# Kernel tuning notes

Measured on AMD Instinct MI355X. Metric: run time of the kernel, lower is better.

## Reference

```python
import jax, jax.numpy as jnp
import numpy as np
from jax import lax

HEAD_NUM = 16
QKV_DIM = 16
TOP_K = 2
SQRT_EMBED = 16.0   # sqrt_embedding_dim for E=256
LOGIT_CLIP = 10.0


def setup_inputs() -> dict:
    key = jax.random.key(0)
    ks = jax.random.split(key, 12)
    B, P, N1, E, HD, NE = 256, 100, 101, 256, 256, 8
    s = 0.05
    return {
        "encoded_last_node": jax.random.normal(ks[0], (B, P, E), jnp.float32),
        "attr": jax.random.uniform(ks[1], (B, P, 4), jnp.float32),
        "encoded_nodes": jax.random.normal(ks[2], (B, N1, E), jnp.float32),
        "ninf_mask": jnp.zeros((B, P, N1), jnp.float32),
        "attention_bias": jax.random.normal(ks[3], (B, P, N1), jnp.float32),
        "attention_bias1": jax.random.normal(ks[4], (B, P, N1), jnp.float32),
        "Wq_last": jax.random.normal(ks[5], (E + 4, HD), jnp.float32) * s,
        "Wk": jax.random.normal(ks[6], (E, HD), jnp.float32) * s,
        "Wv": jax.random.normal(ks[7], (E, HD), jnp.float32) * s,
        "Wg": jax.random.normal(ks[8], (HD, NE), jnp.float32) * s,
        "expert_W": jax.random.normal(ks[9], (NE, HD, E), jnp.float32) * s,
        "expert_b": jnp.zeros((NE, E), jnp.float32),
    }


def _heads(x, H, D):
    B, n, _ = x.shape
    return x.reshape(B, n, H, D).transpose(0, 2, 1, 3)  # (B,H,n,D)


def reference(encoded_last_node, attr, encoded_nodes, ninf_mask,
              attention_bias, attention_bias1, Wq_last, Wk, Wv,
              Wg, expert_W, expert_b):
    B, P, E = encoded_last_node.shape
    H, D = HEAD_NUM, QKV_DIM
    # q from [last_node ; attr], k/v from encoded_nodes (set_kv)
    q = _heads(jnp.concatenate([encoded_last_node, attr], axis=-1) @ Wq_last, H, D)
    k = _heads(encoded_nodes @ Wk, H, D)   # (B,H,N+1,D)
    v = _heads(encoded_nodes @ Wv, H, D)
    inv_sqrt_d = 1.0 / jnp.sqrt(jnp.asarray(D, jnp.float32))
    score = jnp.einsum('bhpd,bhnd->bhpn', q, k) * inv_sqrt_d
    score = score + ninf_mask[:, None, :, :]           # rank3 ninf mask
    w = jax.nn.softmax(score, axis=-1)
    out = jnp.einsum('bhpn,bhnd->bhpd', w, v)
    out_concat = out.transpose(0, 2, 1, 3).reshape(B, P, H * D)
    # --- top-k gated MoE combine (node-level routing, eval path) ---
    x = out_concat.reshape(B * P, H * D)               # tokens
    logits = x @ Wg                                    # (T, NE)
    top_v, top_i = lax.top_k(logits, TOP_K)
    top_g = jax.nn.softmax(top_v, axis=-1)
    gates = jnp.zeros_like(logits).at[
        jnp.arange(x.shape[0])[:, None], top_i].set(top_g)   # (T, NE)
    expert_out = jnp.einsum('tf,efo->teo', x, expert_W) + expert_b[None]
    mh = jnp.einsum('teo,te->to', expert_out, gates).reshape(B, P, E)
    # --- single-head pointer scores with bias + tanh clipping ---
    score2 = jnp.einsum('bpe,bne->bpn', mh, encoded_nodes)
    score2 = score2 + attention_bias + attention_bias1
    score2 = LOGIT_CLIP * jnp.tanh(score2 / SQRT_EMBED)
    probs = jax.nn.softmax(score2 + ninf_mask, axis=-1)  # (B,P,N+1)
    return probs
```

## Files before the change

### kernel.cpp

```cpp
#include <hip/hip_runtime.h>
#include <hip/hip_bf16.h>

#define B   256
#define P   100
#define N1  101
#define E   256
#define HD  256
#define H   16
#define D   16
#define NE  8
#define NTOK (B*P)
#define NKV  (B*N1)

typedef __attribute__((ext_vector_type(8))) short short8;
typedef __attribute__((ext_vector_type(4))) float f32x4;
typedef unsigned short ushort_t;

__device__ __forceinline__ unsigned short f2bf(float f) {
  unsigned int u = __float_as_uint(f);
  unsigned int r = (u + 0x7fffu + ((u >> 16) & 1u)) >> 16;
  return (unsigned short)r;
}
__device__ __forceinline__ float bf2f(unsigned short b) {
  return __uint_as_float(((unsigned int)b) << 16);
}

__global__ __launch_bounds__(256) void wsplit3_kernel(
    const float* __restrict__ W, uint4* __restrict__ Wp, int Kreal) {
  const int gid = blockIdx.x * 256 + threadIdx.x;
  const int lane = gid & 63;
  const int rest = gid >> 6;
  const int gct = rest & 15;
  const int kt = rest >> 4;
  const int k0 = kt * 32 + (lane >> 4) * 8;
  const int c = gct * 16 + (lane & 15);
  unsigned int hw[4], mw[4], lw[4];
#pragma unroll
  for (int jj = 0; jj < 4; ++jj) {
    int ka = k0 + 2 * jj, kb = ka + 1;
    float va = (ka < Kreal) ? W[(size_t)ka * 256 + c] : 0.f;
    float vb = (kb < Kreal) ? W[(size_t)kb * 256 + c] : 0.f;
    unsigned short ha = f2bf(va), hb = f2bf(vb);
    float ra = va - bf2f(ha), rb = vb - bf2f(hb);
    unsigned short ma = f2bf(ra), mb = f2bf(rb);
    unsigned short la = f2bf(ra - bf2f(ma)), lb = f2bf(rb - bf2f(mb));
    hw[jj] = (unsigned int)ha | ((unsigned int)hb << 16);
    mw[jj] = (unsigned int)ma | ((unsigned int)mb << 16);
    lw[jj] = (unsigned int)la | ((unsigned int)lb << 16);
  }
  uint4 uh, um, ul;
  uh.x = hw[0]; uh.y = hw[1]; uh.z = hw[2]; uh.w = hw[3];
  um.x = mw[0]; um.y = mw[1]; um.z = mw[2]; um.w = mw[3];
  ul.x = lw[0]; ul.y = lw[1]; ul.z = lw[2]; ul.w = lw[3];
  Wp[(size_t)(rest * 3 + 0) * 64 + lane] = uh;
  Wp[(size_t)(rest * 3 + 1) * 64 + lane] = um;
  Wp[(size_t)(rest * 3 + 2) * 64 + lane] = ul;
}

__device__ __forceinline__ void split3_pack(const float* v, uint4& uh,
                                            uint4& um, uint4& ul) {
  unsigned int hw[4], mw[4], lw[4];
#pragma unroll
  for (int jj = 0; jj < 4; ++jj) {
    float va = v[2 * jj], vb = v[2 * jj + 1];
    unsigned short ha = f2bf(va), hb = f2bf(vb);
    float ra = va - bf2f(ha), rb = vb - bf2f(hb);
    unsigned short ma = f2bf(ra), mb = f2bf(rb);
    unsigned short la = f2bf(ra - bf2f(ma)), lb = f2bf(rb - bf2f(mb));
    hw[jj] = (unsigned int)ha | ((unsigned int)hb << 16);
    mw[jj] = (unsigned int)ma | ((unsigned int)mb << 16);
    lw[jj] = (unsigned int)la | ((unsigned int)lb << 16);
  }
  uh.x = hw[0]; uh.y = hw[1]; uh.z = hw[2]; uh.w = hw[3];
  um.x = mw[0]; um.y = mw[1]; um.z = mw[2]; um.w = mw[3];
  ul.x = lw[0]; ul.y = lw[1]; ul.z = lw[2]; ul.w = lw[3];
}

__global__ __launch_bounds__(256) void kvproj3_kernel(
    const float* __restrict__ enc, const uint4* __restrict__ Wk3,
    const uint4* __restrict__ Wv3, float* __restrict__ kout,
    float* __restrict__ vout) {
  const int KT = 8;
  const int NKG = KT * 4;
  const int RSTRIDE = KT * 12 + 1;
  __shared__ uint4 als[32 * 97];
  const int tid = threadIdx.x;
  const int row0 = blockIdx.x * 32;
  for (int i = tid; i < 32 * NKG; i += 256) {
    const int row = i >> 5;
    const int kg = i & 31;
    float v[8];
    const float4* s = (const float4*)(enc + (size_t)(row0 + row) * 256 + kg * 8);
    float4 x0 = s[0], x1 = s[1];
    v[0] = x0.x; v[1] = x0.y; v[2] = x0.z; v[3] = x0.w;
    v[4] = x1.x; v[5] = x1.y; v[6] = x1.z; v[7] = x1.w;
    uint4 uh, um, ul;
    split3_pack(v, uh, um, ul);
    const int slot = row * RSTRIDE + kg;
    als[slot] = uh;
    als[slot + NKG] = um;
    als[slot + 2 * NKG] = ul;
  }
  __syncthreads();
  const int w = tid >> 6;
  const int lane = tid & 63;
  const int lr = lane & 15;
  const int lg4 = lane >> 4;
  f32x4 acck[2][4], accv[2][4];
#pragma unroll
  for (int rt = 0; rt < 2; ++rt)
#pragma unroll
    for (int ct = 0; ct < 4; ++ct) {
      acck[rt][ct] = (f32x4){0.f, 0.f, 0.f, 0.f};
      accv[rt][ct] = (f32x4){0.f, 0.f, 0.f, 0.f};
    }
  for (int kt = 0; kt < KT; ++kt) {
    short8 ah[2], am[2], al[2];
#pragma unroll
    for (int rt = 0; rt < 2; ++rt) {
      const int base = (rt * 16 + lr) * RSTRIDE + kt * 4 + lg4;
      ah[rt] = __builtin_bit_cast(short8, als[base]);
      am[rt] = __builtin_bit_cast(short8, als[base + NKG]);
      al[rt] = __builtin_bit_cast(short8, als[base + 2 * NKG]);
    }
#pragma unroll
    for (int ct = 0; ct < 4; ++ct) {
      const int gct = w * 4 + ct;
      const size_t base = (size_t)((kt * 16 + gct) * 3) * 64 + lane;
      {
        short8 bh = __builtin_bit_cast(short8, Wk3[base]);
        short8 bm = __builtin_bit_cast(short8, Wk3[base + 64]);
        short8 bl = __builtin_bit_cast(short8, Wk3[base + 128]);
#pragma unroll
        for (int rt = 0; rt < 2; ++rt) {
          f32x4 a = acck[rt][ct];
          a = __builtin_amdgcn_mfma_f32_16x16x32_bf16(ah[rt], bh, a, 0, 0, 0);
          a = __builtin_amdgcn_mfma_f32_16x16x32_bf16(ah[rt], bm, a, 0, 0, 0);
          a = __builtin_amdgcn_mfma_f32_16x16x32_bf16(am[rt], bh, a, 0, 0, 0);
          a = __builtin_amdgcn_mfma_f32_16x16x32_bf16(am[rt], bm, a, 0, 0, 0);
          a = __builtin_amdgcn_mfma_f32_16x16x32_bf16(ah[rt], bl, a, 0, 0, 0);
          a = __builtin_amdgcn_mfma_f32_16x16x32_bf16(al[rt], bh, a, 0, 0, 0);
          acck[rt][ct] = a;
        }
      }
      {
        short8 bh = __builtin_bit_cast(short8, Wv3[base]);
        short8 bm = __builtin_bit_cast(short8, Wv3[base + 64]);
        short8 bl = __builtin_bit_cast(short8, Wv3[base + 128]);
#pragma unroll
        for (int rt = 0; rt < 2; ++rt) {
          f32x4 a = accv[rt][ct];
          a = __builtin_amdgcn_mfma_f32_16x16x32_bf16(ah[rt], bh, a, 0, 0, 0);
          a = __builtin_amdgcn_mfma_f32_16x16x32_bf16(ah[rt], bm, a, 0, 0, 0);
          a = __builtin_amdgcn_mfma_f32_16x16x32_bf16(am[rt], bh, a, 0, 0, 0);
          a = __builtin_amdgcn_mfma_f32_16x16x32_bf16(am[rt], bm, a, 0, 0, 0);
          a = __builtin_amdgcn_mfma_f32_16x16x32_bf16(ah[rt], bl, a, 0, 0, 0);
          a = __builtin_amdgcn_mfma_f32_16x16x32_bf16(al[rt], bh, a, 0, 0, 0);
          accv[rt][ct] = a;
        }
      }
    }
  }
#pragma unroll
  for (int rt = 0; rt < 2; ++rt) {
#pragma unroll
    for (int ct = 0; ct < 4; ++ct) {
      const int gct = w * 4 + ct;
#pragma unroll
      for (int reg = 0; reg < 4; ++reg) {
        const int row = row0 + rt * 16 + lg4 * 4 + reg;
        int bb = row / N1, nn = row - bb * N1;
        size_t o = (((size_t)bb * H + gct) * N1 + nn) * D + lr;
        kout[o] = acck[rt][ct][reg];
        vout[o] = accv[rt][ct][reg];
      }
    }
  }
}

template <int KT, int MODE>
__global__ __launch_bounds__(256) void proj3_kernel(
    const float* __restrict__ src, const float* __restrict__ attr,
    const uint4* __restrict__ Wp3, float* __restrict__ outp) {
  const int RSTRIDE = KT * 12 + 1;
  __shared__ uint4 als[32 * (KT * 12 + 1)];
  const int tid = threadIdx.x;
  const int row0 = blockIdx.x * 32;
  const int NKG = KT * 4;
  for (int i = tid; i < 32 * NKG; i += 256) {
    const int row = i / NKG;
    const int kg = i - row * NKG;
    float v[8];
    const int kbase = kg * 8;
    if (MODE == 0 || kbase < 256) {
      const float4* s = (const float4*)(src + (size_t)(row0 + row) * 256 + kbase);
      float4 x0 = s[0], x1 = s[1];
      v[0] = x0.x; v[1] = x0.y; v[2] = x0.z; v[3] = x0.w;
      v[4] = x1.x; v[5] = x1.y; v[6] = x1.z; v[7] = x1.w;
    } else {
#pragma unroll
      for (int j = 0; j < 8; ++j) {
        int k = kbase + j;
        v[j] = (k >= 256 && k < 260) ? attr[(size_t)(row0 + row) * 4 + (k - 256)]
                                     : 0.f;
      }
    }
    uint4 uh, um, ul;
    split3_pack(v, uh, um, ul);
    const int slot = row * RSTRIDE + kg;
    als[slot] = uh;
    als[slot + NKG] = um;
    als[slot + 2 * NKG] = ul;
  }
  __syncthreads();
  const int w = tid >> 6;
  const int lane = tid & 63;
  const int lr = lane & 15;
  const int lg4 = lane >> 4;
  f32x4 acc[2][4];
#pragma unroll
  for (int rt = 0; rt < 2; ++rt)
#pragma unroll
    for (int ct = 0; ct < 4; ++ct) acc[rt][ct] = (f32x4){0.f, 0.f, 0.f, 0.f};
  for (int kt = 0; kt < KT; ++kt) {
    short8 ah[2], am[2], al[2];
#pragma unroll
    for (int rt = 0; rt < 2; ++rt) {
      const int base = (rt * 16 + lr) * RSTRIDE + kt * 4 + lg4;
      ah[rt] = __builtin_bit_cast(short8, als[base]);
      am[rt] = __builtin_bit_cast(short8, als[base + NKG]);
      al[rt] = __builtin_bit_cast(short8, als[base + 2 * NKG]);
    }
#pragma unroll
    for (int ct = 0; ct < 4; ++ct) {
      const int gct = w * 4 + ct;
      const size_t base = (size_t)((kt * 16 + gct) * 3) * 64 + lane;
      short8 bh = __builtin_bit_cast(short8, Wp3[base]);
      short8 bm = __builtin_bit_cast(short8, Wp3[base + 64]);
      short8 bl = __builtin_bit_cast(short8, Wp3[base + 128]);
#pragma unroll
      for (int rt = 0; rt < 2; ++rt) {
        f32x4 a = acc[rt][ct];
        a = __builtin_amdgcn_mfma_f32_16x16x32_bf16(ah[rt], bh, a, 0, 0, 0);
        a = __builtin_amdgcn_mfma_f32_16x16x32_bf16(ah[rt], bm, a, 0, 0, 0);
        a = __builtin_amdgcn_mfma_f32_16x16x32_bf16(am[rt], bh, a, 0, 0, 0);
        a = __builtin_amdgcn_mfma_f32_16x16x32_bf16(am[rt], bm, a, 0, 0, 0);
        a = __builtin_amdgcn_mfma_f32_16x16x32_bf16(ah[rt], bl, a, 0, 0, 0);
        a = __builtin_amdgcn_mfma_f32_16x16x32_bf16(al[rt], bh, a, 0, 0, 0);
        acc[rt][ct] = a;
      }
    }
  }
#pragma unroll
  for (int rt = 0; rt < 2; ++rt) {
#pragma unroll
    for (int ct = 0; ct < 4; ++ct) {
      const int gct = w * 4 + ct;
#pragma unroll
      for (int reg = 0; reg < 4; ++reg) {
        const int row = row0 + rt * 16 + lg4 * 4 + reg;
        size_t o;
        if (MODE == 0) {
          int bb = row / N1, nn = row - bb * N1;
          o = (((size_t)bb * H + gct) * N1 + nn) * D + lr;
        } else {
          int bb = row / P, pp = row - bb * P;
          o = (((size_t)bb * H + gct) * P + pp) * D + lr;
        }
        outp[o] = acc[rt][ct][reg];
      }
    }
  }
}

__device__ __forceinline__ float dot16f(
    const float4& a0, const float4& a1, const float4& a2, const float4& a3,
    const float4& b0, const float4& b1, const float4& b2, const float4& b3) {
  float s = a0.x * b0.x;
  s = fmaf(a0.y, b0.y, s); s = fmaf(a0.z, b0.z, s); s = fmaf(a0.w, b0.w, s);
  s = fmaf(a1.x, b1.x, s); s = fmaf(a1.y, b1.y, s); s = fmaf(a1.z, b1.z, s);
  s = fmaf(a1.w, b1.w, s);
  s = fmaf(a2.x, b2.x, s); s = fmaf(a2.y, b2.y, s); s = fmaf(a2.z, b2.z, s);
  s = fmaf(a2.w, b2.w, s);
  s = fmaf(a3.x, b3.x, s); s = fmaf(a3.y, b3.y, s); s = fmaf(a3.z, b3.z, s);
  s = fmaf(a3.w, b3.w, s);
  return s;
}

__global__ __launch_bounds__(256) void attn_kernel(
    const float* __restrict__ q, const float* __restrict__ k,
    const float* __restrict__ v, const float* __restrict__ ninf,
    float* __restrict__ x) {
  const int b = blockIdx.x >> 3;
  const int h0 = (blockIdx.x & 7) * 2;
  __shared__ float4 kl4[2 * 208];
  __shared__ float4 vl4[2 * 208];
  const int tid = threadIdx.x;
  const int w = tid >> 6;
  const int lane = tid & 63;
  const int hh = w >> 1;
  const int h = h0 + hh;
  const int prow = (w & 1) * 64 + lane;
  const bool act = (prow < P);
  const int p = act ? prow : (P - 1);
  const float LOG2E = 1.4426950408889634f;
  const float c1 = 0.25f * LOG2E;
  const float* qb = q + (((size_t)b * H + h) * P + p) * D;
  float4 qa0 = *(const float4*)&qb[0];
  float4 qa1 = *(const float4*)&qb[4];
  float4 qa2 = *(const float4*)&qb[8];
  float4 qa3 = *(const float4*)&qb[12];
  qa0.x *= c1; qa0.y *= c1; qa0.z *= c1; qa0.w *= c1;
  qa1.x *= c1; qa1.y *= c1; qa1.z *= c1; qa1.w *= c1;
  qa2.x *= c1; qa2.y *= c1; qa2.z *= c1; qa2.w *= c1;
  qa3.x *= c1; qa3.y *= c1; qa3.z *= c1; qa3.w *= c1;
  const float* mrow = ninf + ((size_t)b * P + p) * N1;
  const float* kw = (const float*)(kl4 + hh * 208);
  const float* vw = (const float*)(vl4 + hh * 208);

  float m2 = -1e30f, l = 0.f;
  float o[16];
#pragma unroll
  for (int d = 0; d < 16; ++d) o[d] = 0.f;

#pragma unroll
  for (int ch = 0; ch < 2; ++ch) {
    const int c0 = ch ? 52 : 0;
    const int len = ch ? 49 : 52;
    const int nf4 = len * 4;
    __syncthreads();
    for (int i = tid; i < 2 * nf4; i += 256) {
      int hs = i / nf4, rem = i - hs * nf4;
      const float4* ks =
          (const float4*)(k + (((size_t)b * H + h0 + hs) * N1 + c0) * D);
      const float4* vs =
          (const float4*)(v + (((size_t)b * H + h0 + hs) * N1 + c0) * D);
      kl4[hs * 208 + rem] = ks[rem];
      vl4[hs * 208 + rem] = vs[rem];
    }
    __syncthreads();
    const int nit = len >> 2;
    float4 mk = *(const float4*)&mrow[c0];
    for (int it = 0; it < nit; ++it) {
      const int j = it * 4;
      const int nn = (it < nit - 1) ? (c0 + j + 4) : c0;
      float4 nx = *(const float4*)&mrow[nn];
      const float4* kr0 = (const float4*)&kw[(j + 0) * D];
      const float4* kr1 = (const float4*)&kw[(j + 1) * D];
      const float4* kr2 = (const float4*)&kw[(j + 2) * D];
      const float4* kr3 = (const float4*)&kw[(j + 3) * D];
      float4 k00 = kr0[0], k01 = kr0[1], k02 = kr0[2], k03 = kr0[3];
      float4 k10 = kr1[0], k11 = kr1[1], k12 = kr1[2], k13 = kr1[3];
      float4 k20 = kr2[0], k21 = kr2[1], k22 = kr2[2], k23 = kr2[3];
      float4 k30 = kr3[0], k31 = kr3[1], k32 = kr3[2], k33 = kr3[3];
      float s0 = fmaf(mk.x, LOG2E, dot16f(qa0, qa1, qa2, qa3, k00, k01, k02, k03));
      float s1 = fmaf(mk.y, LOG2E, dot16f(qa0, qa1, qa2, qa3, k10, k11, k12, k13));
      float s2 = fmaf(mk.z, LOG2E, dot16f(qa0, qa1, qa2, qa3, k20, k21, k22, k23));
      float s3 = fmaf(mk.w, LOG2E, dot16f(qa0, qa1, qa2, qa3, k30, k31, k32, k33));
      float mn = fmaxf(fmaxf(fmaxf(s0, s1), fmaxf(s2, s3)), m2);
      float sc = exp2f(m2 - mn);
      float p0 = exp2f(s0 - mn), p1 = exp2f(s1 - mn);
      float p2 = exp2f(s2 - mn), p3 = exp2f(s3 - mn);
      l = fmaf(l, sc, (p0 + p1) + (p2 + p3));
      const float4* vr0 = (const float4*)&vw[(j + 0) * D];
      const float4* vr1 = (const float4*)&vw[(j + 1) * D];
      const float4* vr2 = (const float4*)&vw[(j + 2) * D];
      const float4* vr3 = (const float4*)&vw[(j + 3) * D];
#pragma unroll
      for (int dq = 0; dq < 4; ++dq) {
        float4 v0 = vr0[dq], v1 = vr1[dq], v2 = vr2[dq], v3 = vr3[dq];
        o[4 * dq + 0] = fmaf(o[4 * dq + 0], sc,
            fmaf(p0, v0.x, fmaf(p1, v1.x, fmaf(p2, v2.x, p3 * v3.x))));
        o[4 * dq + 1] = fmaf(o[4 * dq + 1], sc,
            fmaf(p0, v0.y, fmaf(p1, v1.y, fmaf(p2, v2.y, p3 * v3.y))));
        o[4 * dq + 2] = fmaf(o[4 * dq + 2], sc,
            fmaf(p0, v0.z, fmaf(p1, v1.z, fmaf(p2, v2.z, p3 * v3.z))));
        o[4 * dq + 3] = fmaf(o[4 * dq + 3], sc,
            fmaf(p0, v0.w, fmaf(p1, v1.w, fmaf(p2, v2.w, p3 * v3.w))));
      }
      m2 = mn;
      mk = nx;
    }
  }
  {
    const float tm = mrow[100];
    const float4* kr = (const float4*)&kw[48 * D];
    float4 k0 = kr[0], k1 = kr[1], k2 = kr[2], k3 = kr[3];
    float s = fmaf(tm, LOG2E, dot16f(qa0, qa1, qa2, qa3, k0, k1, k2, k3));
    float mn = fmaxf(m2, s);
    float sc = exp2f(m2 - mn);
    float pp = exp2f(s - mn);
    l = fmaf(l, sc, pp);
    const float4* vr = (const float4*)&vw[48 * D];
#pragma unroll
    for (int dq = 0; dq < 4; ++dq) {
      float4 v0 = vr[dq];
      o[4 * dq + 0] = fmaf(o[4 * dq + 0], sc, pp * v0.x);
      o[4 * dq + 1] = fmaf(o[4 * dq + 1], sc, pp * v0.y);
      o[4 * dq + 2] = fmaf(o[4 * dq + 2], sc, pp * v0.z);
      o[4 * dq + 3] = fmaf(o[4 * dq + 3], sc, pp * v0.w);
    }
  }
  if (act) {
    const float inv = 1.f / l;
    float* xr = &x[((size_t)b * P + p) * HD + h * D];
#pragma unroll
    for (int dq = 0; dq < 4; ++dq) {
      float4 t;
      t.x = o[4 * dq + 0] * inv; t.y = o[4 * dq + 1] * inv;
      t.z = o[4 * dq + 2] * inv; t.w = o[4 * dq + 3] * inv;
      *(float4*)&xr[4 * dq] = t;
    }
  }
}

__global__ __launch_bounds__(256) void logits_top2_kernel(
    const float* __restrict__ x, const float* __restrict__ Wg,
    int* __restrict__ topi, float* __restrict__ topg,
    ushort_t* __restrict__ xsplit) {
  __shared__ float xl[32][260];
  __shared__ float wg[E * NE];
  __shared__ float lg[32][9];
  const int tid = threadIdx.x;
  const int t0 = blockIdx.x * 32;
  for (int r = 0; r < 32; ++r) {
    float val = x[(size_t)(t0 + r) * HD + tid];
    xl[r][tid] = val;
    unsigned short hi = f2bf(val);
    unsigned short lo = f2bf(val - bf2f(hi));
    xsplit[(size_t)(t0 + r) * 512 + tid] = hi;
    xsplit[(size_t)(t0 + r) * 512 + 256 + tid] = lo;
  }
  for (int i = tid; i < E * NE; i += 256) wg[i] = Wg[i];
  __syncthreads();
  const int r = tid >> 3, e = tid & 7;
  float acc = 0.f;
  for (int f = 0; f < E; ++f) acc += xl[r][f] * wg[f * NE + e];
  lg[r][e] = acc;
  __syncthreads();
  if (tid < 32) {
    float v[8];
#pragma unroll
    for (int j = 0; j < 8; ++j) v[j] = lg[tid][j];
    int i1 = 0; float v1 = v[0];
#pragma unroll
    for (int j = 1; j < 8; ++j) if (v[j] > v1) { v1 = v[j]; i1 = j; }
    int i2 = -1; float v2 = -1e30f;
#pragma unroll
    for (int j = 0; j < 8; ++j)
      if (j != i1 && v[j] > v2) { v2 = v[j]; i2 = j; }
    float ex = __expf(v2 - v1);
    float g1 = 1.f / (1.f + ex);
    float g2 = ex / (1.f + ex);
    int t = t0 + tid;
    topi[t * 2 + 0] = i1; topi[t * 2 + 1] = i2;
    topg[t * 2 + 0] = g1; topg[t * 2 + 1] = g2;
  }
}

__global__ __launch_bounds__(1024) void build_lists_kernel(
    const int* __restrict__ topi, const float* __restrict__ topg,
    int* __restrict__ list_tok, float* __restrict__ list_gate,
    int* __restrict__ counts) {
  const int e = blockIdx.x;
  const int tid = threadIdx.x;
  const int lane = tid & 63, w = tid >> 6;
  __shared__ int wsum[16];
  int running = 0;
  for (int c = 0; c < NTOK; c += 1024) {
    int t = c + tid;
    int ia = topi[t * 2 + 0], ib = topi[t * 2 + 1];
    int slot = (ia == e) ? 0 : ((ib == e) ? 1 : -1);
    int f = (slot >= 0) ? 1 : 0;
    unsigned long long m = __ballot(f);
    if (lane == 0) wsum[w] = __popcll(m);
    __syncthreads();
    int wbase = 0, total = 0;
#pragma unroll
    for (int i = 0; i < 16; ++i) {
      int s = wsum[i];
      if (i < w) wbase += s;
      total += s;
    }
    if (f) {
      int prefix = __popcll(m & ((1ull << lane) - 1ull));
      int pos = running + wbase + prefix;
      list_tok[e * NTOK + pos] = (t << 1) | slot;
      list_gate[e * NTOK + pos] = topg[t * 2 + slot];
    }
    running += total;
    __syncthreads();
  }
  if (tid == 0) counts[e] = running;
}

__global__ __launch_bounds__(256) void wsplit_kernel(
    const float* __restrict__ eW, uint4* __restrict__ Wp) {
  const int gid = blockIdx.x * 256 + threadIdx.x;
  const int lane = gid & 63;
  const int rest = gid >> 6;
  const int gct = rest & 15;
  const int kt = (rest >> 4) & 7;
  const int e = rest >> 7;
  const int kbase = kt * 32 + (lane >> 4) * 8;
  const int c = gct * 16 + (lane & 15);
  unsigned int hi[4], lo[4];
#pragma unroll
  for (int jj = 0; jj < 4; ++jj) {
    float v0 = eW[((size_t)e * HD + (kbase + 2 * jj)) * E + c];
    float v1 = eW[((size_t)e * HD + (kbase + 2 * jj + 1)) * E + c];
    unsigned short h0 = f2bf(v0), h1 = f2bf(v1);
    unsigned short l0 = f2bf(v0 - bf2f(h0)), l1 = f2bf(v1 - bf2f(h1));
    hi[jj] = (unsigned int)h0 | ((unsigned int)h1 << 16);
    lo[jj] = (unsigned int)l0 | ((unsigned int)l1 << 16);
  }
  uint4 uh, ul;
  uh.x = hi[0]; uh.y = hi[1]; uh.z = hi[2]; uh.w = hi[3];
  ul.x = lo[0]; ul.y = lo[1]; ul.z = lo[2]; ul.w = lo[3];
  Wp[(size_t)(rest * 2 + 0) * 64 + lane] = uh;
  Wp[(size_t)(rest * 2 + 1) * 64 + lane] = ul;
}

__global__ __launch_bounds__(256) void expert_gemm_kernel(
    const ushort_t* __restrict__ xsplit, const uint4* __restrict__ Wp,
    const float* __restrict__ eb, const int* __restrict__ list_tok,
    const float* __restrict__ list_gate, const int* __restrict__ counts,
    float* __restrict__ p0, float* __restrict__ p1) {
  int e = 0, t0 = -1;
  {
    int rem = blockIdx.x;
    for (int i = 0; i < NE; ++i) {
      int nt = (counts[i] + 31) >> 5;
      if (rem < nt) { e = i; t0 = rem * 32; break; }
      rem -= nt;
    }
  }
  if (t0 < 0) return;
  const int cnt = counts[e];
  const int nr = min(32, cnt - t0);
  __shared__ uint4 xls[32 * 65];
  __shared__ int stok[32];
  __shared__ float sg[32];
  const int tid = threadIdx.x;
  if (tid < 32) {
    int src = e * NTOK + t0 + ((tid < nr) ? tid : 0);
    stok[tid] = list_tok[src];
    sg[tid] = (tid < nr) ? list_gate[e * NTOK + t0 + tid] : 0.f;
  }
  __syncthreads();
  for (int i = tid; i < 32 * 64; i += 256) {
    int r = i >> 6, ch = i & 63;
    const uint4* src = (const uint4*)(xsplit + (size_t)(stok[r] >> 1) * 512);
    xls[r * 65 + ch] = src[ch];
  }
  __syncthreads();
  const int w = tid >> 6;
  const int lane = tid & 63;
  const int lr = lane & 15;
  const int lg4 = lane >> 4;
  f32x4 acc[2][4];
#pragma unroll
  for (int rt = 0; rt < 2; ++rt)
#pragma unroll
    for (int ct = 0; ct < 4; ++ct) acc[rt][ct] = (f32x4){0.f, 0.f, 0.f, 0.f};

  for (int kt = 0; kt < 8; ++kt) {
    short8 afrag[2][2];
#pragma unroll
    for (int rt = 0; rt < 2; ++rt)
#pragma unroll
      for (int pl = 0; pl < 2; ++pl) {
        uint4 u = xls[(rt * 16 + lr) * 65 + pl * 32 + kt * 4 + lg4];
        afrag[rt][pl] = __builtin_bit_cast(short8, u);
      }
#pragma unroll
    for (int ct = 0; ct < 4; ++ct) {
      const int gct = w * 4 + ct;
      const size_t base = (size_t)(((e * 8 + kt) * 16 + gct) * 2) * 64 + lane;
      short8 bh = __builtin_bit_cast(short8, Wp[base]);
      short8 bl = __builtin_bit_cast(short8, Wp[base + 64]);
#pragma unroll
      for (int rt = 0; rt < 2; ++rt) {
        acc[rt][ct] = __builtin_amdgcn_mfma_f32_16x16x32_bf16(
            afrag[rt][0], bh, acc[rt][ct], 0, 0, 0);
        acc[rt][ct] = __builtin_amdgcn_mfma_f32_16x16x32_bf16(
            afrag[rt][0], bl, acc[rt][ct], 0, 0, 0);
        acc[rt][ct] = __builtin_amdgcn_mfma_f32_16x16x32_bf16(
            afrag[rt][1], bh, acc[rt][ct], 0, 0, 0);
      }
    }
  }
#pragma unroll
  for (int rt = 0; rt < 2; ++rt) {
#pragma unroll
    for (int ct = 0; ct < 4; ++ct) {
      const int col = (w * 4 + ct) * 16 + lr;
      const float bias = eb[e * E + col];
#pragma unroll
      for (int reg = 0; reg < 4; ++reg) {
        const int ridx = rt * 16 + lg4 * 4 + reg;
        if (ridx < nr) {
          const int tokw = stok[ridx];
          const float g = sg[ridx];
          float* dst = ((tokw & 1) ? p1 : p0) + (size_t)(tokw >> 1) * E + col;
          *dst = g * (acc[rt][ct][reg] + bias);
        }
      }
    }
  }
}

__global__ __launch_bounds__(128) void score2_kernel(
    const float* __restrict__ p0, const float* __restrict__ p1,
    const float* __restrict__ enc, float* __restrict__ out) {
  const int b = blockIdx.y;
  const int pt = blockIdx.x * 25;
  __shared__ float mh[25][E];
  const int tid = threadIdx.x;
  for (int i = tid; i < 25 * E; i += 128) {
    int r = i >> 8, c = i & 255;
    int t = b * P + pt + r;
    mh[r][c] = p0[(size_t)t * E + c] + p1[(size_t)t * E + c];
  }
  __syncthreads();
  const int n = tid;
  if (n >= N1) return;
  float acc[25];
#pragma unroll
  for (int r = 0; r < 25; ++r) acc[r] = 0.f;
  const float* er = enc + ((size_t)b * N1 + n) * E;
  for (int ee = 0; ee < E; ee += 4) {
    float4 ev = *(const float4*)&er[ee];
#pragma unroll
    for (int r = 0; r < 25; ++r) {
      float4 mv = *(const float4*)&mh[r][ee];
      acc[r] += mv.x * ev.x + mv.y * ev.y + mv.z * ev.z + mv.w * ev.w;
    }
  }
#pragma unroll
  for (int r = 0; r < 25; ++r) out[((size_t)b * P + pt + r) * N1 + n] = acc[r];
}

__global__ __launch_bounds__(256) void softmax2_kernel(
    float* __restrict__ sc, const float* __restrict__ ab,
    const float* __restrict__ ab1, const float* __restrict__ ninf) {
  const int row = blockIdx.x * 4 + (threadIdx.x >> 6);
  const int lane = threadIdx.x & 63;
  float* srow = sc + (size_t)row * N1;
  const float* a = ab + (size_t)row * N1;
  const float* a1 = ab1 + (size_t)row * N1;
  const float* nf = ninf + (size_t)row * N1;
  float s0 = -1e30f, s1 = -1e30f;
  {
    int i = lane;
    float s = srow[i] + a[i] + a1[i];
    float e2 = __expf(s * 0.125f);
    float th = 1.f - 2.f / (e2 + 1.f);
    s0 = 10.f * th + nf[i];
  }
  if (lane < N1 - 64) {
    int i = lane + 64;
    float s = srow[i] + a[i] + a1[i];
    float e2 = __expf(s * 0.125f);
    float th = 1.f - 2.f / (e2 + 1.f);
    s1 = 10.f * th + nf[i];
  }
  float mx = fmaxf(s0, s1);
#pragma unroll
  for (int off = 32; off > 0; off >>= 1) mx = fmaxf(mx, __shfl_xor(mx, off, 64));
  float p0 = __expf(s0 - mx);
  float p1 = (lane < N1 - 64) ? __expf(s1 - mx) : 0.f;
  float sum = p0 + p1;
#pragma unroll
  for (int off = 32; off > 0; off >>= 1) sum += __shfl_xor(sum, off, 64);
  float inv = 1.f / sum;
  srow[lane] = p0 * inv;
  if (lane < N1 - 64) srow[lane + 64] = p1 * inv;
}

extern "C" void kernel_launch(void* const* d_in, const int* in_sizes, int n_in,
                              void* d_out, int out_size, void* d_ws,
                              size_t ws_size, hipStream_t stream) {
  const float* eln  = (const float*)d_in[0];
  const float* attr = (const float*)d_in[1];
  const float* enc  = (const float*)d_in[2];
  const float* ninf = (const float*)d_in[3];
  const float* ab   = (const float*)d_in[4];
  const float* ab1  = (const float*)d_in[5];
  const float* Wq   = (const float*)d_in[6];
  const float* Wk   = (const float*)d_in[7];
  const float* Wv   = (const float*)d_in[8];
  const float* Wg   = (const float*)d_in[9];
  const float* eW   = (const float*)d_in[10];
  const float* eb   = (const float*)d_in[11];
  float* out = (float*)d_out;

  char* ws = (char*)d_ws;
  size_t off = 0;
  auto carve = [&](size_t bytes) {
    char* p = ws + off;
    off += (bytes + 255) & ~size_t(255);
    return p;
  };
  float* kbuf = (float*)carve(sizeof(float) * NKV * HD);
  float* vbuf = (float*)carve(sizeof(float) * NKV * HD);
  float* qbuf = (float*)carve(sizeof(float) * NTOK * HD);
  float* xbuf = (float*)carve(sizeof(float) * NTOK * HD);
  int*   topi = (int*)carve(sizeof(int) * NTOK * 2);
  float* topg = (float*)carve(sizeof(float) * NTOK * 2);
  int*   counts = (int*)carve(sizeof(int) * 16);
  int*   list_tok = (int*)carve(sizeof(int) * NE * NTOK);
  float* list_gate = (float*)carve(sizeof(float) * NE * NTOK);
  uint4* Wp  = (uint4*)carve(sizeof(ushort_t) * NE * HD * E * 2);
  uint4* Wk3 = (uint4*)carve((size_t)8 * 16 * 3 * 64 * 16);
  uint4* Wv3 = (uint4*)carve((size_t)8 * 16 * 3 * 64 * 16);
  uint4* Wq3 = (uint4*)carve((size_t)9 * 16 * 3 * 64 * 16);
  float* pp0 = kbuf;
  float* pp1 = vbuf;
  ushort_t* xsplit = (ushort_t*)qbuf;

  wsplit_kernel<<<256, 256, 0, stream>>>(eW, Wp);
  wsplit3_kernel<<<32, 256, 0, stream>>>(Wk, Wk3, 256);
  wsplit3_kernel<<<32, 256, 0, stream>>>(Wv, Wv3, 256);
  wsplit3_kernel<<<36, 256, 0, stream>>>(Wq, Wq3, 260);
  kvproj3_kernel<<<NKV / 32, 256, 0, stream>>>(enc, Wk3, Wv3, kbuf, vbuf);
  proj3_kernel<9, 1><<<NTOK / 32, 256, 0, stream>>>(eln, attr, Wq3, qbuf);
  attn_kernel<<<B * 8, 256, 0, stream>>>(qbuf, kbuf, vbuf, ninf, xbuf);
  logits_top2_kernel<<<NTOK / 32, 256, 0, stream>>>(xbuf, Wg, topi, topg,
                                                    xsplit);
  build_lists_kernel<<<NE, 1024, 0, stream>>>(topi, topg, list_tok, list_gate,
                                              counts);
  expert_gemm_kernel<<<1608, 256, 0, stream>>>(xsplit, Wp, eb, list_tok,
                                               list_gate, counts, pp0, pp1);
  dim3 s2(4, B);
  score2_kernel<<<s2, 128, 0, stream>>>(pp0, pp1, enc, out);
  softmax2_kernel<<<NTOK / 4, 256, 0, stream>>>(out, ab, ab1, ninf);
}
```

Baseline: 327.1 us.

## Use hardware bf16 pack conversion and load full K/V into shared memory once

Replaces the software round-to-nearest bf16 split with the v_cvt_pk_bf16_f32 instruction in the weight and activation split helpers. In attention, all 101 K/V rows for both heads are staged into LDS at once, replacing the two-chunk load with its extra barriers. Hardware conversion cuts ALU work per split. Single staging removes a sync and a reload at the cost of roughly double the LDS per block, which may lower occupancy.

```diff
diff --git a/kernel.cpp b/kernel.cpp
--- a/kernel.cpp
+++ b/kernel.cpp
@@ -24,6 +24,35 @@
 __device__ __forceinline__ float bf2f(unsigned short b) {
   return __uint_as_float(((unsigned int)b) << 16);
 }
+__device__ __forceinline__ unsigned int cvtpk(float a, float b) {
+  unsigned int r;
+  asm("v_cvt_pk_bf16_f32 %0, %1, %2" : "=v"(r) : "v"(a), "v"(b));
+  return r;
+}
+__device__ __forceinline__ float lo2f(unsigned int u) {
+  return __uint_as_float(u << 16);
+}
+__device__ __forceinline__ float hi2f(unsigned int u) {
+  return __uint_as_float(u & 0xffff0000u);
+}
+
+__device__ __forceinline__ void split3_pack(const float* v, uint4& uh,
+                                            uint4& um, uint4& ul) {
+  unsigned int hw[4], mw[4], lw[4];
+#pragma unroll
+  for (int jj = 0; jj < 4; ++jj) {
+    float va = v[2 * jj], vb = v[2 * jj + 1];
+    unsigned int h = cvtpk(va, vb);
+    float ra = va - lo2f(h), rb = vb - hi2f(h);
+    unsigned int m = cvtpk(ra, rb);
+    float sa = ra - lo2f(m), sb = rb - hi2f(m);
+    unsigned int l = cvtpk(sa, sb);
+    hw[jj] = h; mw[jj] = m; lw[jj] = l;
+  }
+  uh.x = hw[0]; uh.y = hw[1]; uh.z = hw[2]; uh.w = hw[3];
+  um.x = mw[0]; um.y = mw[1]; um.z = mw[2]; um.w = mw[3];
+  ul.x = lw[0]; ul.y = lw[1]; ul.z = lw[2]; ul.w = lw[3];
+}
 
 __global__ __launch_bounds__(256) void wsplit3_kernel(
     const float* __restrict__ W, uint4* __restrict__ Wp, int Kreal) {
@@ -34,46 +63,17 @@
   const int kt = rest >> 4;
   const int k0 = kt * 32 + (lane >> 4) * 8;
   const int c = gct * 16 + (lane & 15);
-  unsigned int hw[4], mw[4], lw[4];
-#pragma unroll
-  for (int jj = 0; jj < 4; ++jj) {
-    int ka = k0 + 2 * jj, kb = ka + 1;
-    float va = (ka < Kreal) ? W[(size_t)ka * 256 + c] : 0.f;
-    float vb = (kb < Kreal) ? W[(size_t)kb * 256 + c] : 0.f;
-    unsigned short ha = f2bf(va), hb = f2bf(vb);
-    float ra = va - bf2f(ha), rb = vb - bf2f(hb);
-    unsigned short ma = f2bf(ra), mb = f2bf(rb);
-    unsigned short la = f2bf(ra - bf2f(ma)), lb = f2bf(rb - bf2f(mb));
-    hw[jj] = (unsigned int)ha | ((unsigned int)hb << 16);
-    mw[jj] = (unsigned int)ma | ((unsigned int)mb << 16);
-    lw[jj] = (unsigned int)la | ((unsigned int)lb << 16);
+  float v[8];
+#pragma unroll
+  for (int j = 0; j < 8; ++j) {
+    int kk = k0 + j;
+    v[j] = (kk < Kreal) ? W[(size_t)kk * 256 + c] : 0.f;
   }
   uint4 uh, um, ul;
-  uh.x = hw[0]; uh.y = hw[1]; uh.z = hw[2]; uh.w = hw[3];
-  um.x = mw[0]; um.y = mw[1]; um.z = mw[2]; um.w = mw[3];
-  ul.x = lw[0]; ul.y = lw[1]; ul.z = lw[2]; ul.w = lw[3];
+  split3_pack(v, uh, um, ul);
   Wp[(size_t)(rest * 3 + 0) * 64 + lane] = uh;
   Wp[(size_t)(rest * 3 + 1) * 64 + lane] = um;
   Wp[(size_t)(rest * 3 + 2) * 64 + lane] = ul;
-}
-
-__device__ __forceinline__ void split3_pack(const float* v, uint4& uh,
-                                            uint4& um, uint4& ul) {
-  unsigned int hw[4], mw[4], lw[4];
-#pragma unroll
-  for (int jj = 0; jj < 4; ++jj) {
-    float va = v[2 * jj], vb = v[2 * jj + 1];
-    unsigned short ha = f2bf(va), hb = f2bf(vb);
-    float ra = va - bf2f(ha), rb = vb - bf2f(hb);
-    unsigned short ma = f2bf(ra), mb = f2bf(rb);
-    unsigned short la = f2bf(ra - bf2f(ma)), lb = f2bf(rb - bf2f(mb));
-    hw[jj] = (unsigned int)ha | ((unsigned int)hb << 16);
-    mw[jj] = (unsigned int)ma | ((unsigned int)mb << 16);
-    lw[jj] = (unsigned int)la | ((unsigned int)lb << 16);
-  }
-  uh.x = hw[0]; uh.y = hw[1]; uh.z = hw[2]; uh.w = hw[3];
-  um.x = mw[0]; um.y = mw[1]; um.z = mw[2]; um.w = mw[3];
-  ul.x = lw[0]; ul.y = lw[1]; ul.z = lw[2]; ul.w = lw[3];
 }
 
 __global__ __launch_bounds__(256) void kvproj3_kernel(
@@ -293,9 +293,17 @@
     float* __restrict__ x) {
   const int b = blockIdx.x >> 3;
   const int h0 = (blockIdx.x & 7) * 2;
-  __shared__ float4 kl4[2 * 208];
-  __shared__ float4 vl4[2 * 208];
+  __shared__ float4 kl4[2 * N1 * 4];
+  __shared__ float4 vl4[2 * N1 * 4];
   const int tid = threadIdx.x;
+  {
+    const float4* ks = (const float4*)(k + ((size_t)b * H + h0) * N1 * D);
+    const float4* vs = (const float4*)(v + ((size_t)b * H + h0) * N1 * D);
+    for (int i = tid; i < 2 * N1 * 4; i += 256) {
+      kl4[i] = ks[i];
+      vl4[i] = vs[i];
+    }
+  }
   const int w = tid >> 6;
   const int lane = tid & 63;
   const int hh = w >> 1;
@@ -315,83 +323,66 @@
   qa2.x *= c1; qa2.y *= c1; qa2.z *= c1; qa2.w *= c1;
   qa3.x *= c1; qa3.y *= c1; qa3.z *= c1; qa3.w *= c1;
   const float* mrow = ninf + ((size_t)b * P + p) * N1;
-  const float* kw = (const float*)(kl4 + hh * 208);
-  const float* vw = (const float*)(vl4 + hh * 208);
+  const float* kw = (const float*)(kl4 + hh * N1 * 4);
+  const float* vw = (const float*)(vl4 + hh * N1 * 4);
+  __syncthreads();
 
   float m2 = -1e30f, l = 0.f;
   float o[16];
 #pragma unroll
   for (int d = 0; d < 16; ++d) o[d] = 0.f;
-
-#pragma unroll
-  for (int ch = 0; ch < 2; ++ch) {
-    const int c0 = ch ? 52 : 0;
-    const int len = ch ? 49 : 52;
-    const int nf4 = len * 4;
-    __syncthreads();
-    for (int i = tid; i < 2 * nf4; i += 256) {
-      int hs = i / nf4, rem = i - hs * nf4;
-      const float4* ks =
-          (const float4*)(k + (((size_t)b * H + h0 + hs) * N1 + c0) * D);
-      const float4* vs =
-          (const float4*)(v + (((size_t)b * H + h0 + hs) * N1 + c0) * D);
-      kl4[hs * 208 + rem] = ks[rem];
-      vl4[hs * 208 + rem] = vs[rem];
-    }
-    __syncthreads();
-    const int nit = len >> 2;
-    float4 mk = *(const float4*)&mrow[c0];
-    for (int it = 0; it < nit; ++it) {
-      const int j = it * 4;
-      const int nn = (it < nit - 1) ? (c0 + j + 4) : c0;
-      float4 nx = *(const float4*)&mrow[nn];
-      const float4* kr0 = (const float4*)&kw[(j + 0) * D];
-      const float4* kr1 = (const float4*)&kw[(j + 1) * D];
-      const float4* kr2 = (const float4*)&kw[(j + 2) * D];
-      const float4* kr3 = (const float4*)&kw[(j + 3) * D];
-      float4 k00 = kr0[0], k01 = kr0[1], k02 = kr0[2], k03 = kr0[3];
-      float4 k10 = kr1[0], k11 = kr1[1], k12 = kr1[2], k13 = kr1[3];
-      float4 k20 = kr2[0], k21 = kr2[1], k22 = kr2[2], k23 = kr2[3];
-      float4 k30 = kr3[0], k31 = kr3[1], k32 = kr3[2], k33 = kr3[3];
-      float s0 = fmaf(mk.x, LOG2E, dot16f(qa0, qa1, qa2, qa3, k00, k01, k02, k03));
-      float s1 = fmaf(mk.y, LOG2E, dot16f(qa0, qa1, qa2, qa3, k10, k11, k12, k13));
-      float s2 = fmaf(mk.z, LOG2E, dot16f(qa0, qa1, qa2, qa3, k20, k21, k22, k23));
-      float s3 = fmaf(mk.w, LOG2E, dot16f(qa0, qa1, qa2, qa3, k30, k31, k32, k33));
-      float mn = fmaxf(fmaxf(fmaxf(s0, s1), fmaxf(s2, s3)), m2);
-      float sc = exp2f(m2 - mn);
-      float p0 = exp2f(s0 - mn), p1 = exp2f(s1 - mn);
-      float p2 = exp2f(s2 - mn), p3 = exp2f(s3 - mn);
-      l = fmaf(l, sc, (p0 + p1) + (p2 + p3));
-      const float4* vr0 = (const float4*)&vw[(j + 0) * D];
-      const float4* vr1 = (const float4*)&vw[(j + 1) * D];
-      const float4* vr2 = (const float4*)&vw[(j + 2) * D];
-      const float4* vr3 = (const float4*)&vw[(j + 3) * D];
-#pragma unroll
-      for (int dq = 0; dq < 4; ++dq) {
-        float4 v0 = vr0[dq], v1 = vr1[dq], v2 = vr2[dq], v3 = vr3[dq];
-        o[4 * dq + 0] = fmaf(o[4 * dq + 0], sc,
-            fmaf(p0, v0.x, fmaf(p1, v1.x, fmaf(p2, v2.x, p3 * v3.x))));
-        o[4 * dq + 1] = fmaf(o[4 * dq + 1], sc,
-            fmaf(p0, v0.y, fmaf(p1, v1.y, fmaf(p2, v2.y, p3 * v3.y))));
-        o[4 * dq + 2] = fmaf(o[4 * dq + 2], sc,
-            fmaf(p0, v0.z, fmaf(p1, v1.z, fmaf(p2, v2.z, p3 * v3.z))));
-        o[4 * dq + 3] = fmaf(o[4 * dq + 3], sc,
-            fmaf(p0, v0.w, fmaf(p1, v1.w, fmaf(p2, v2.w, p3 * v3.w))));
-      }
-      m2 = mn;
-      mk = nx;
-    }
+  float4 mk = *(const float4*)&mrow[0];
+  const float tmask = mrow[100];
+
+  for (int it = 0; it < 25; ++it) {
+    const int j = it * 4;
+    const int nn = (it < 24) ? (j + 4) : 0;
+    float4 nx = *(const float4*)&mrow[nn];
+    const float4* kr0 = (const float4*)&kw[(j + 0) * D];
+    const float4* kr1 = (const float4*)&kw[(j + 1) * D];
+    const float4* kr2 = (const float4*)&kw[(j + 2) * D];
+    const float4* kr3 = (const float4*)&kw[(j + 3) * D];
+    float4 k00 = kr0[0], k01 = kr0[1], k02 = kr0[2], k03 = kr0[3];
+    float4 k10 = kr1[0], k11 = kr1[1], k12 = kr1[2], k13 = kr1[3];
+    float4 k20 = kr2[0], k21 = kr2[1], k22 = kr2[2], k23 = kr2[3];
+    float4 k30 = kr3[0], k31 = kr3[1], k32 = kr3[2], k33 = kr3[3];
+    float s0 = fmaf(mk.x, LOG2E, dot16f(qa0, qa1, qa2, qa3, k00, k01, k02, k03));
+    float s1 = fmaf(mk.y, LOG2E, dot16f(qa0, qa1, qa2, qa3, k10, k11, k12, k13));
+    float s2 = fmaf(mk.z, LOG2E, dot16f(qa0, qa1, qa2, qa3, k20, k21, k22, k23));
+    float s3 = fmaf(mk.w, LOG2E, dot16f(qa0, qa1, qa2, qa3, k30, k31, k32, k33));
+    float mn = fmaxf(fmaxf(fmaxf(s0, s1), fmaxf(s2, s3)), m2);
+    float sc = exp2f(m2 - mn);
+    float p0 = exp2f(s0 - mn), p1 = exp2f(s1 - mn);
+    float p2 = exp2f(s2 - mn), p3 = exp2f(s3 - mn);
+    l = fmaf(l, sc, (p0 + p1) + (p2 + p3));
+    const float4* vr0 = (const float4*)&vw[(j + 0) * D];
+    const float4* vr1 = (const float4*)&vw[(j + 1) * D];
+    const float4* vr2 = (const float4*)&vw[(j + 2) * D];
+    const float4* vr3 = (const float4*)&vw[(j + 3) * D];
+#pragma unroll
+    for (int dq = 0; dq < 4; ++dq) {
+      float4 v0 = vr0[dq], v1 = vr1[dq], v2 = vr2[dq], v3 = vr3[dq];
+      o[4 * dq + 0] = fmaf(o[4 * dq + 0], sc,
+          fmaf(p0, v0.x, fmaf(p1, v1.x, fmaf(p2, v2.x, p3 * v3.x))));
+      o[4 * dq + 1] = fmaf(o[4 * dq + 1], sc,
+          fmaf(p0, v0.y, fmaf(p1, v1.y, fmaf(p2, v2.y, p3 * v3.y))));
+      o[4 * dq + 2] = fmaf(o[4 * dq + 2], sc,
+          fmaf(p0, v0.z, fmaf(p1, v1.z, fmaf(p2, v2.z, p3 * v3.z))));
+      o[4 * dq + 3] = fmaf(o[4 * dq + 3], sc,
+          fmaf(p0, v0.w, fmaf(p1, v1.w, fmaf(p2, v2.w, p3 * v3.w))));
+    }
+    m2 = mn;
+    mk = nx;
   }
   {
-    const float tm = mrow[100];
-    const float4* kr = (const float4*)&kw[48 * D];
+    const float4* kr = (const float4*)&kw[100 * D];
     float4 k0 = kr[0], k1 = kr[1], k2 = kr[2], k3 = kr[3];
-    float s = fmaf(tm, LOG2E, dot16f(qa0, qa1, qa2, qa3, k0, k1, k2, k3));
+    float s = fmaf(tmask, LOG2E, dot16f(qa0, qa1, qa2, qa3, k0, k1, k2, k3));
     float mn = fmaxf(m2, s);
     float sc = exp2f(m2 - mn);
     float pp = exp2f(s - mn);
     l = fmaf(l, sc, pp);
-    const float4* vr = (const float4*)&vw[48 * D];
+    const float4* vr = (const float4*)&vw[100 * D];
 #pragma unroll
     for (int dq = 0; dq < 4; ++dq) {
       float4 v0 = vr[dq];
@@ -509,10 +500,10 @@
   for (int jj = 0; jj < 4; ++jj) {
     float v0 = eW[((size_t)e * HD + (kbase + 2 * jj)) * E + c];
     float v1 = eW[((size_t)e * HD + (kbase + 2 * jj + 1)) * E + c];
-    unsigned short h0 = f2bf(v0), h1 = f2bf(v1);
-    unsigned short l0 = f2bf(v0 - bf2f(h0)), l1 = f2bf(v1 - bf2f(h1));
-    hi[jj] = (unsigned int)h0 | ((unsigned int)h1 << 16);
-    lo[jj] = (unsigned int)l0 | ((unsigned int)l1 << 16);
+    unsigned int h = cvtpk(v0, v1);
+    float r0 = v0 - lo2f(h), r1 = v1 - hi2f(h);
+    unsigned int l = cvtpk(r0, r1);
+    hi[jj] = h; lo[jj] = l;
   }
   uint4 uh, ul;
   uh.x = hi[0]; uh.y = hi[1]; uh.z = hi[2]; uh.w = hi[3];
```

Result: no change. 328.3 us (+0.4%).
